# Performance work log

Measured on AMD Instinct MI355X. Metric: run time of the kernel, lower is better.

Reference implementation:

```python
import jax, jax.numpy as jnp
import numpy as np

N = 10000      # nodes
E = 160000     # edges
K = 32         # MC samples (dim 1 of inputs)
D_IN = 128
D_OUT = 32


def setup_inputs() -> dict:
    key = jax.random.key(0)
    k1, k2, k3, k4, k5 = jax.random.split(key, 5)
    x = jax.random.normal(k1, (N, K, D_IN), dtype=jnp.float32)
    # Glorot-uniform weight as in weight_variable_glorot
    init_range = np.sqrt(6.0 / (D_IN + D_OUT))
    weights = jax.random.uniform(k2, (D_IN, D_OUT), dtype=jnp.float32,
                                 minval=-init_range, maxval=init_range)
    edge_row = jax.random.randint(k3, (E,), 0, N, dtype=jnp.int32)
    edge_col = jax.random.randint(k4, (E,), 0, N, dtype=jnp.int32)
    edge_val = jax.random.uniform(k5, (E,), dtype=jnp.float32)
    return {"x": x, "weights": weights, "edge_row": edge_row,
            "edge_col": edge_col, "edge_val": edge_val}


def reference(x, weights, edge_row, edge_col, edge_val):
    # Original loops over K slices doing: dropout(p=0) -> x @ W -> spmm(adj, x) -> relu,
    # then concatenates along axis 1. Batched equivalent:
    h = jnp.einsum('nkd,de->nke', x, weights)            # [N, K, D_OUT]
    # sparse adj @ h : out[r] += val * h[c] for each edge (r, c, val)
    msg = h[edge_col] * edge_val[:, None, None]          # [E, K, D_OUT]
    agg = jax.ops.segment_sum(msg, edge_row, num_segments=N)  # [N, K, D_OUT]
    return jax.nn.relu(agg)
```

## Files before the change

### kernel.cpp

```cpp
#include <hip/hip_runtime.h>
#include <hip/hip_bf16.h>

#define KK 32
#define DIN 128
#define DOUT 32
#define NVEC (KK * DOUT)
#define NV4  (NVEC / 4)
#define MBKT 64
#define OCAP 4096
#define TROWS 128

typedef float        vf4 __attribute__((ext_vector_type(4)));
typedef unsigned int vu4 __attribute__((ext_vector_type(4)));

__device__ __forceinline__ float bfu2f(unsigned int u) {
    return __uint_as_float(u << 16);
}
__device__ __forceinline__ unsigned int f2bfu(float f) {
    __hip_bfloat16 b = __float2bfloat16(f);
    return *(unsigned short*)&b;
}

__global__ __launch_bounds__(256) void gemm_kernel(
    const float* __restrict__ x, const float* __restrict__ w,
    unsigned short* __restrict__ h)
{
    __shared__ vf4 xl[TROWS * 32];
    __shared__ vf4 wl[DIN * DOUT / 4];
    const int tid = threadIdx.x;

    const vf4* w4 = (const vf4*)w;
    #pragma unroll
    for (int i = tid; i < DIN * DOUT / 4; i += 256) wl[i] = w4[i];

    const vf4* x4 = (const vf4*)x + (size_t)blockIdx.x * (TROWS * 32);
    #pragma unroll
    for (int k = 0; k < (TROWS * 32) / 256; ++k) {
        int f = tid + k * 256;
        int r = f >> 5;
        int g = f & 31;
        xl[r * 32 + (g ^ ((r >> 2) & 7))] = x4[f];
    }
    __syncthreads();

    const int eg  = tid & 7;
    const int rg  = tid >> 3;
    const int rg8 = rg & 7;
    const int r0  = blockIdx.x * TROWS + rg * 4;

    float acc[4][4];
    #pragma unroll
    for (int a = 0; a < 4; ++a)
        #pragma unroll
        for (int b = 0; b < 4; ++b) acc[a][b] = 0.f;

    #pragma unroll 2
    for (int d4 = 0; d4 < DIN / 4; ++d4) {
        vf4 wv0 = wl[(d4 * 4 + 0) * 8 + eg];
        vf4 wv1 = wl[(d4 * 4 + 1) * 8 + eg];
        vf4 wv2 = wl[(d4 * 4 + 2) * 8 + eg];
        vf4 wv3 = wl[(d4 * 4 + 3) * 8 + eg];
        #pragma unroll
        for (int rr = 0; rr < 4; ++rr) {
            vf4 xv = xl[(rg * 4 + rr) * 32 + (d4 ^ rg8)];
            acc[rr][0] += xv.x * wv0.x + xv.y * wv1.x + xv.z * wv2.x + xv.w * wv3.x;
            acc[rr][1] += xv.x * wv0.y + xv.y * wv1.y + xv.z * wv2.y + xv.w * wv3.y;
            acc[rr][2] += xv.x * wv0.z + xv.y * wv1.z + xv.z * wv2.z + xv.w * wv3.z;
            acc[rr][3] += xv.x * wv0.w + xv.y * wv1.w + xv.z * wv2.w + xv.w * wv3.w;
        }
    }
    #pragma unroll
    for (int rr = 0; rr < 4; ++rr) {
        uint2 packed;
        packed.x = f2bfu(acc[rr][0]) | (f2bfu(acc[rr][1]) << 16);
        packed.y = f2bfu(acc[rr][2]) | (f2bfu(acc[rr][3]) << 16);
        *(uint2*)(h + (size_t)(r0 + rr) * DOUT + eg * 4) = packed;
    }
}

__global__ void zero_kernel(int* __restrict__ p, int n) {
    int i = blockIdx.x * 256 + threadIdx.x;
    if (i < n) p[i] = 0;
}

__global__ void fill_bucket_kernel(
    const int* __restrict__ row, const int* __restrict__ col,
    const float* __restrict__ val, int* __restrict__ cursor,
    uint2* __restrict__ bedge,
    int* __restrict__ ocnt, int* __restrict__ orow,
    int* __restrict__ ocol, float* __restrict__ oval, int E)
{
    int i = blockIdx.x * 256 + threadIdx.x;
    if (i >= E) return;
    int r = row[i];
    int p = atomicAdd(&cursor[r], 1);
    if (p < MBKT) {
        uint2 e;
        e.x = (unsigned int)col[i];
        e.y = __float_as_uint(val[i]);
        bedge[r * MBKT + p] = e;
    } else {
        int q = atomicAdd(ocnt, 1);
        if (q < OCAP) {
            orow[q] = r;
            ocol[q] = col[i];
            oval[q] = val[i];
        }
    }
}

__global__ __launch_bounds__(256) void agg_kernel(
    const unsigned short* __restrict__ h, const int* __restrict__ cursor,
    const uint2* __restrict__ bedge,
    const int* __restrict__ ocnt, const int* __restrict__ orow,
    const int* __restrict__ ocol, const float* __restrict__ oval,
    float* __restrict__ out)
{
    const int tid  = threadIdx.x;
    const int half = tid >> 7;
    const int lt   = tid & 127;
    const int lane = tid & 63;
    const int r    = blockIdx.x * 2 + half;

    const int deg  = cursor[r];
    const int degb = deg < MBKT ? deg : MBKT;

    int   ec = 0;
    float ev = 0.f;
    if (lane < degb) {
        uint2 e = bedge[r * MBKT + lane];
        ec = (int)e.x;
        ev = __uint_as_float(e.y);
    }

    float acc[8];
    #pragma unroll
    for (int q = 0; q < 8; ++q) acc[q] = 0.f;

    #pragma unroll 4
    for (int j = 0; j < degb; ++j) {
        int   c = __shfl(ec, j, 64);
        float v = __shfl(ev, j, 64);
        vu4 p = *(const vu4*)(h + (size_t)c * NVEC + lt * 8);
        acc[0] += v * bfu2f(p.x & 0xffffu);
        acc[1] += v * bfu2f(p.x >> 16);
        acc[2] += v * bfu2f(p.y & 0xffffu);
        acc[3] += v * bfu2f(p.y >> 16);
        acc[4] += v * bfu2f(p.z & 0xffffu);
        acc[5] += v * bfu2f(p.z >> 16);
        acc[6] += v * bfu2f(p.w & 0xffffu);
        acc[7] += v * bfu2f(p.w >> 16);
    }

    int on = *ocnt;
    if (on > 0) {
        if (on > OCAP) on = OCAP;
        for (int q = 0; q < on; ++q) {
            if (orow[q] == r) {
                int   c = ocol[q];
                float v = oval[q];
                vu4 p = *(const vu4*)(h + (size_t)c * NVEC + lt * 8);
                acc[0] += v * bfu2f(p.x & 0xffffu);
                acc[1] += v * bfu2f(p.x >> 16);
                acc[2] += v * bfu2f(p.y & 0xffffu);
                acc[3] += v * bfu2f(p.y >> 16);
                acc[4] += v * bfu2f(p.z & 0xffffu);
                acc[5] += v * bfu2f(p.z >> 16);
                acc[6] += v * bfu2f(p.w & 0xffffu);
                acc[7] += v * bfu2f(p.w >> 16);
            }
        }
    }

    vf4 o0, o1;
    o0.x = fmaxf(acc[0], 0.f); o0.y = fmaxf(acc[1], 0.f);
    o0.z = fmaxf(acc[2], 0.f); o0.w = fmaxf(acc[3], 0.f);
    o1.x = fmaxf(acc[4], 0.f); o1.y = fmaxf(acc[5], 0.f);
    o1.z = fmaxf(acc[6], 0.f); o1.w = fmaxf(acc[7], 0.f);
    vf4* op = (vf4*)out + (size_t)r * NV4 + lt * 2;
    __builtin_nontemporal_store(o0, &op[0]);
    __builtin_nontemporal_store(o1, &op[1]);
}

extern "C" void kernel_launch(void* const* d_in, const int* in_sizes, int n_in,
                              void* d_out, int out_size, void* d_ws, size_t ws_size,
                              hipStream_t stream)
{
    const float* x    = (const float*)d_in[0];
    const float* w    = (const float*)d_in[1];
    const int*   erow = (const int*)d_in[2];
    const int*   ecol = (const int*)d_in[3];
    const float* eval = (const float*)d_in[4];
    float* out = (float*)d_out;

    const int E = in_sizes[2];
    const int N = in_sizes[0] / (KK * DIN);
    const int R = N * KK;

    char* ws = (char*)d_ws;
    size_t off = 0;
    auto take = [&](size_t bytes) {
        void* p = ws + off;
        off += (bytes + 15) & ~(size_t)15;
        return p;
    };
    unsigned short* h = (unsigned short*)take((size_t)R * DOUT * sizeof(unsigned short));
    int*   cursor = (int*)take((size_t)(N + 1) * sizeof(int));
    uint2* bedge  = (uint2*)take((size_t)N * MBKT * sizeof(uint2));
    int*   orow   = (int*)take((size_t)OCAP * sizeof(int));
    int*   ocol   = (int*)take((size_t)OCAP * sizeof(int));
    float* oval   = (float*)take((size_t)OCAP * sizeof(float));
    int*   ocnt   = cursor + N;
    (void)ws_size;

    gemm_kernel<<<R / TROWS, 256, 0, stream>>>(x, w, h);
    zero_kernel<<<(N + 1 + 255) / 256, 256, 0, stream>>>(cursor, N + 1);
    fill_bucket_kernel<<<(E + 255) / 256, 256, 0, stream>>>(
        erow, ecol, eval, cursor, bedge, ocnt, orow, ocol, oval, E);
    agg_kernel<<<N / 2, 256, 0, stream>>>(
        h, cursor, bedge, ocnt, orow, ocol, oval, out);
}
```

Baseline: 314.9 us.

## Compute dense projection with bf16 MFMA instead of FP32 FMA loops

Result: faster. 305.9 us (-2.8%).

```diff
diff --git a/kernel.cpp b/kernel.cpp
--- a/kernel.cpp
+++ b/kernel.cpp
@@ -8,10 +8,10 @@
 #define NV4  (NVEC / 4)
 #define MBKT 64
 #define OCAP 4096
-#define TROWS 128
-
-typedef float        vf4 __attribute__((ext_vector_type(4)));
-typedef unsigned int vu4 __attribute__((ext_vector_type(4)));
+
+typedef float        vf4   __attribute__((ext_vector_type(4)));
+typedef unsigned int vu4   __attribute__((ext_vector_type(4)));
+typedef short        bf16x8 __attribute__((ext_vector_type(8)));
 
 __device__ __forceinline__ float bfu2f(unsigned int u) {
     return __uint_as_float(u << 16);
@@ -25,56 +25,71 @@
     const float* __restrict__ x, const float* __restrict__ w,
     unsigned short* __restrict__ h)
 {
-    __shared__ vf4 xl[TROWS * 32];
-    __shared__ vf4 wl[DIN * DOUT / 4];
-    const int tid = threadIdx.x;
-
-    const vf4* w4 = (const vf4*)w;
+    __shared__ float cbuf[4][16 * 33];
+    const int tid  = threadIdx.x;
+    const int lane = tid & 63;
+    const int wid  = tid >> 6;
+    const int q    = lane >> 4;
+    const int lm   = lane & 15;
+
+    bf16x8 bf[2][4];
     #pragma unroll
-    for (int i = tid; i < DIN * DOUT / 4; i += 256) wl[i] = w4[i];
-
-    const vf4* x4 = (const vf4*)x + (size_t)blockIdx.x * (TROWS * 32);
+    for (int nt = 0; nt < 2; ++nt) {
+        #pragma unroll
+        for (int ks = 0; ks < 4; ++ks) {
+            bf16x8 f;
+            #pragma unroll
+            for (int j = 0; j < 8; ++j) {
+                int k = ks * 32 + q * 8 + j;
+                f[j] = (short)f2bfu(w[k * DOUT + nt * 16 + lm]);
+            }
+            bf[nt][ks] = f;
+        }
+    }
+
+    const int wgid = blockIdx.x * 4 + wid;
+    float* cb = &cbuf[wid][0];
+
     #pragma unroll
-    for (int k = 0; k < (TROWS * 32) / 256; ++k) {
-        int f = tid + k * 256;
-        int r = f >> 5;
-        int g = f & 31;
-        xl[r * 32 + (g ^ ((r >> 2) & 7))] = x4[f];
-    }
-    __syncthreads();
-
-    const int eg  = tid & 7;
-    const int rg  = tid >> 3;
-    const int rg8 = rg & 7;
-    const int r0  = blockIdx.x * TROWS + rg * 4;
-
-    float acc[4][4];
-    #pragma unroll
-    for (int a = 0; a < 4; ++a)
+    for (int it = 0; it < 2; ++it) {
+        const int tile = wgid * 2 + it;
+        const int r0   = tile * 16;
+        const float* xrow = x + (size_t)(r0 + lm) * DIN + q * 8;
+
+        vf4 acc0 = {0.f, 0.f, 0.f, 0.f};
+        vf4 acc1 = {0.f, 0.f, 0.f, 0.f};
+
         #pragma unroll
-        for (int b = 0; b < 4; ++b) acc[a][b] = 0.f;
-
-    #pragma unroll 2
-    for (int d4 = 0; d4 < DIN / 4; ++d4) {
-        vf4 wv0 = wl[(d4 * 4 + 0) * 8 + eg];
-        vf4 wv1 = wl[(d4 * 4 + 1) * 8 + eg];
-        vf4 wv2 = wl[(d4 * 4 + 2) * 8 + eg];
-        vf4 wv3 = wl[(d4 * 4 + 3) * 8 + eg];
+        for (int ks = 0; ks < 4; ++ks) {
+            vf4 a0 = *(const vf4*)(xrow + ks * 32);
+            vf4 a1 = *(const vf4*)(xrow + ks * 32 + 4);
+            bf16x8 af;
+            af[0] = (short)f2bfu(a0.x); af[1] = (short)f2bfu(a0.y);
+            af[2] = (short)f2bfu(a0.z); af[3] = (short)f2bfu(a0.w);
+            af[4] = (short)f2bfu(a1.x); af[5] = (short)f2bfu(a1.y);
+            af[6] = (short)f2bfu(a1.z); af[7] = (short)f2bfu(a1.w);
+            acc0 = __builtin_amdgcn_mfma_f32_16x16x32_bf16(af, bf[0][ks], acc0, 0, 0, 0);
+            acc1 = __builtin_amdgcn_mfma_f32_16x16x32_bf16(af, bf[1][ks], acc1, 0, 0, 0);
+        }
+
         #pragma unroll
-        for (int rr = 0; rr < 4; ++rr) {
-            vf4 xv = xl[(rg * 4 + rr) * 32 + (d4 ^ rg8)];
-            acc[rr][0] += xv.x * wv0.x + xv.y * wv1.x + xv.z * wv2.x + xv.w * wv3.x;
-            acc[rr][1] += xv.x * wv0.y + xv.y * wv1.y + xv.z * wv2.y + xv.w * wv3.y;
-            acc[rr][2] += xv.x * wv0.z + xv.y * wv1.z + xv.z * wv2.z + xv.w * wv3.z;
-            acc[rr][3] += xv.x * wv0.w + xv.y * wv1.w + xv.z * wv2.w + xv.w * wv3.w;
-        }
-    }
-    #pragma unroll
-    for (int rr = 0; rr < 4; ++rr) {
-        uint2 packed;
-        packed.x = f2bfu(acc[rr][0]) | (f2bfu(acc[rr][1]) << 16);
-        packed.y = f2bfu(acc[rr][2]) | (f2bfu(acc[rr][3]) << 16);
-        *(uint2*)(h + (size_t)(r0 + rr) * DOUT + eg * 4) = packed;
+        for (int q2 = 0; q2 < 4; ++q2) {
+            int row = q * 4 + q2;
+            cb[row * 33 + lm]      = acc0[q2];
+            cb[row * 33 + 16 + lm] = acc1[q2];
+        }
+        __syncthreads();
+
+        const int rr = lane >> 2;
+        const int cs = (lane & 3) * 8;
+        const float* src = cb + rr * 33 + cs;
+        vu4 packed;
+        packed.x = f2bfu(src[0]) | (f2bfu(src[1]) << 16);
+        packed.y = f2bfu(src[2]) | (f2bfu(src[3]) << 16);
+        packed.z = f2bfu(src[4]) | (f2bfu(src[5]) << 16);
+        packed.w = f2bfu(src[6]) | (f2bfu(src[7]) << 16);
+        *(vu4*)(h + (size_t)(r0 + rr) * DOUT + cs) = packed;
+        __syncthreads();
     }
 }
 
@@ -213,7 +228,7 @@
     int*   ocnt   = cursor + N;
     (void)ws_size;
 
-    gemm_kernel<<<R / TROWS, 256, 0, stream>>>(x, w, h);
+    gemm_kernel<<<R / 128, 256, 0, stream>>>(x, w, h);
     zero_kernel<<<(N + 1 + 255) / 256, 256, 0, stream>>>(cursor, N + 1);
     fill_bucket_kernel<<<(E + 255) / 256, 256, 0, stream>>>(
         erow, ecol, eval, cursor, bedge, ocnt, orow, ocol, oval, E);
```
